# Optimization experiments

Hardware: AMD Instinct MI355X
Metric: run time of the kernel (lower is better)

Reference implementation:

```python
import jax, jax.numpy as jnp
import numpy as np

B, S, IN, H, T, OUT = 128, 336, 64, 1024, 96, 1


def _lstm_step(h, c, x, W_ih, W_hh, b_ih, b_hh):
    # PyTorch LSTM cell: gates in (i, f, g, o) order
    g = x @ W_ih.T + b_ih + h @ W_hh.T + b_hh  # [B, 4H]
    i, f, gg, o = jnp.split(g, 4, axis=-1)
    c_new = jax.nn.sigmoid(f) * c + jax.nn.sigmoid(i) * jnp.tanh(gg)
    h_new = jax.nn.sigmoid(o) * jnp.tanh(c_new)
    return h_new, c_new


def setup_inputs() -> dict:
    key = jax.random.key(0)
    ks = jax.random.split(key, 12)
    s = 0.05
    return {
        "src": jax.random.normal(ks[0], (B, S, IN), jnp.float32),
        "enc_W_ih": jax.random.normal(ks[1], (4 * H, IN), jnp.float32) * s,
        "enc_W_hh": jax.random.normal(ks[2], (4 * H, H), jnp.float32) * s,
        "enc_b_ih": jax.random.normal(ks[3], (4 * H,), jnp.float32) * s,
        "enc_b_hh": jax.random.normal(ks[4], (4 * H,), jnp.float32) * s,
        "dec_W_ih": jax.random.normal(ks[5], (4 * H, OUT + H), jnp.float32) * s,
        "dec_W_hh": jax.random.normal(ks[6], (4 * H, H), jnp.float32) * s,
        "dec_b_ih": jax.random.normal(ks[7], (4 * H,), jnp.float32) * s,
        "dec_b_hh": jax.random.normal(ks[8], (4 * H,), jnp.float32) * s,
        "attn_W": jax.random.normal(ks[9], (H, H), jnp.float32) * s,
        "fc_W": jax.random.normal(ks[10], (OUT, H), jnp.float32) * s,
        "fc_b": jax.random.normal(ks[11], (OUT,), jnp.float32) * s,
        "target_len": T,
    }


def reference(src, enc_W_ih, enc_W_hh, enc_b_ih, enc_b_hh,
              dec_W_ih, dec_W_hh, dec_b_ih, dec_b_hh,
              attn_W, fc_W, fc_b, target_len):
    batch = src.shape[0]
    hdim = enc_W_hh.shape[1]

    # ---- Encoder: single-layer LSTM over src, batch_first ----
    def enc_step(carry, x_t):
        h, c = carry
        h, c = _lstm_step(h, c, x_t, enc_W_ih, enc_W_hh, enc_b_ih, enc_b_hh)
        return (h, c), h

    h0 = jnp.zeros((batch, hdim), src.dtype)
    c0 = jnp.zeros((batch, hdim), src.dtype)
    (h_enc, c_enc), enc_hs = jax.lax.scan(enc_step, (h0, c0),
                                          jnp.swapaxes(src, 0, 1))
    encoder_outputs = jnp.swapaxes(enc_hs, 0, 1)  # [B, S, H]

    def dec_step(carry, _):
        h, c, prev_y = carry
        q = h @ attn_W.T                                      # [B, H]
        energy = jnp.einsum('bh,bsh->bs', q, encoder_outputs)  # [B, S]
        w = jax.nn.softmax(energy, axis=-1)
        ctx = jnp.einsum('bs,bsh->bh', w, encoder_outputs)     # [B, H]
        x = jnp.concatenate([prev_y, ctx], axis=-1)            # [B, OUT+H]
        h, c = _lstm_step(h, c, x, dec_W_ih, dec_W_hh, dec_b_ih, dec_b_hh)
        pred = h @ fc_W.T + fc_b                               # [B, OUT]
        prev_y = jax.lax.stop_gradient(pred)                   # pred.detach()
        return (h, c, prev_y), pred

    prev_y0 = jnp.zeros((batch, fc_W.shape[0]), src.dtype)
    _, preds = jax.lax.scan(dec_step, (h_enc, c_enc, prev_y0), None,
                            length=target_len)
    return jnp.swapaxes(preds, 0, 1)  # [B, target_len, OUT]
```

## Files before the change

kernel.cpp:

```cpp
#include <hip/hip_runtime.h>
#include <math.h>

#define Bn   128
#define Sn   336
#define INd  64
#define Hn   1024
#define Tn   96
#define G4   4096
#define KCE  34
#define KCD  65
#define KCQ  32

typedef __attribute__((ext_vector_type(8))) short short8;
typedef __attribute__((ext_vector_type(4))) float floatx4;
typedef __attribute__((ext_vector_type(4))) unsigned int uintx4;

__device__ __forceinline__ float sigmoidf_(float x){ return 1.0f/(1.0f+expf(-x)); }

__device__ __forceinline__ unsigned short f2bf(float f){
    union { float f; unsigned u; } v; v.f = f;
    unsigned r = v.u + 0x7fffu + ((v.u >> 16) & 1u);
    return (unsigned short)(r >> 16);
}
__device__ __forceinline__ float bflo(unsigned u){ union{unsigned u; float f;} v; v.u = u << 16;        return v.f; }
__device__ __forceinline__ float bfhi(unsigned u){ union{unsigned u; float f;} v; v.u = u & 0xffff0000u; return v.f; }
__device__ __forceinline__ void unpack8v(uintx4 v, float* f){
    f[0]=bflo(v.x); f[1]=bfhi(v.x); f[2]=bflo(v.y); f[3]=bfhi(v.y);
    f[4]=bflo(v.z); f[5]=bfhi(v.z); f[6]=bflo(v.w); f[7]=bfhi(v.w);
}

__global__ void pack_encf(const float* __restrict__ Wih, const float* __restrict__ Whh,
                          const float* __restrict__ bih, const float* __restrict__ bhh,
                          unsigned short* __restrict__ Wp, float* __restrict__ bc){
    long n = (long)256*KCE*512;
    for (long idx = (long)blockIdx.x*256 + threadIdx.x; idx < n; idx += (long)gridDim.x*256){
        int j = (int)(idx & 7), l = (int)((idx >> 3) & 63);
        int kc = (int)((idx >> 9) % KCE);
        int s  = (int)(idx / (KCE*512));
        int c = l & 15, kg = l >> 4;
        int k = kc*32 + kg*8 + j;
        int gate = s & 3, unit = (s >> 2)*16 + c;
        int orig = gate*Hn + unit;
        float v = (k < INd) ? Wih[orig*INd + k] : Whh[(size_t)orig*Hn + (k - INd)];
        Wp[idx] = f2bf(v);
    }
    int tid = blockIdx.x*256 + threadIdx.x;
    if (tid < G4){
        int g = (tid >> 4) & 3, u = (tid >> 6)*16 + (tid & 15);
        int orig = g*Hn + u;
        bc[tid] = bih[orig] + bhh[orig];
    }
}

__global__ void pack_decf(const float* __restrict__ Wih, const float* __restrict__ Whh,
                          const float* __restrict__ bih, const float* __restrict__ bhh,
                          unsigned short* __restrict__ Wp, float* __restrict__ bc){
    long n = (long)256*KCD*512;
    for (long idx = (long)blockIdx.x*256 + threadIdx.x; idx < n; idx += (long)gridDim.x*256){
        int j = (int)(idx & 7), l = (int)((idx >> 3) & 63);
        int kc = (int)((idx >> 9) % KCD);
        int s  = (int)(idx / (KCD*512));
        int c = l & 15, kg = l >> 4;
        int k = kc*32 + kg*8 + j;
        int gate = s & 3, unit = (s >> 2)*16 + c;
        int orig = gate*Hn + unit;
        float v;
        if (k < Hn)          v = Wih[(size_t)orig*(Hn+1) + 1 + k];
        else if (k < 2*Hn)   v = Whh[(size_t)orig*Hn + (k - Hn)];
        else if (k == 2*Hn)  v = Wih[(size_t)orig*(Hn+1)];
        else                 v = 0.0f;
        Wp[idx] = f2bf(v);
    }
    int tid = blockIdx.x*256 + threadIdx.x;
    if (tid < G4){
        int g = (tid >> 4) & 3, u = (tid >> 6)*16 + (tid & 15);
        int orig = g*Hn + u;
        bc[tid] = bih[orig] + bhh[orig];
    }
}

__global__ void pack_attnf(const float* __restrict__ w, unsigned short* __restrict__ Wp){
    int n = 64*KCQ*512;
    for (int idx = blockIdx.x*256 + threadIdx.x; idx < n; idx += gridDim.x*256){
        int j = idx & 7, l = (idx >> 3) & 63;
        int kc = (idx >> 9) & 31;
        int s  = idx >> 14;
        int nn = s*16 + (l & 15);
        int k = kc*32 + (l >> 4)*8 + j;
        Wp[idx] = f2bf(w[(size_t)nn*Hn + k]);
    }
}

__global__ void conv_srcf(const float* __restrict__ s, unsigned short* __restrict__ d){
    int n = Sn*8*2*512;
    for (int idx = blockIdx.x*256 + threadIdx.x; idx < n; idx += gridDim.x*256){
        int j = idx & 7, l = (idx >> 3) & 63;
        int kc = (idx >> 9) & 1, rg = (idx >> 10) & 7, t = idx >> 13;
        int b = rg*16 + (l & 15);
        int k = kc*32 + (l >> 4)*8 + j;
        d[idx] = f2bf(s[((size_t)b*Sn + t)*INd + k]);
    }
}

__global__ void init_ws(unsigned short* __restrict__ hf0, float* __restrict__ cbuf,
                        unsigned short* __restrict__ A0, unsigned short* __restrict__ A1){
    for (int i = blockIdx.x*256 + threadIdx.x; i < 8*KCD*512; i += gridDim.x*256){
        A0[i] = 0; A1[i] = 0;
        if (i < 8*32*512) hf0[i] = 0;
        if (i < Bn*Hn) cbuf[i] = 0.0f;
    }
}

__device__ __forceinline__ void swz(int b, int& x, int& y){
    int xcd = b & 7, li = b >> 3;
    y = xcd*8 + (li & 7);
    x = li >> 3;
}

__global__ __launch_bounds__(256)
void enc_step(const unsigned short* __restrict__ srcfrag,
              const unsigned short* __restrict__ hin,
              const unsigned short* __restrict__ Wf,
              const float* __restrict__ bc, float* __restrict__ cbuf,
              unsigned short* __restrict__ hout,
              unsigned short* __restrict__ enco,
              unsigned short* __restrict__ adec0,
              int t, int last)
{
    __shared__ float red[2][16][65];
    const int tid = threadIdx.x, l = tid & 63, w = tid >> 6;
    const int rgw = w & 1, kh = w >> 1;
    int x, y; swz(blockIdx.x, x, y);
    const int rg = x*2 + rgw;
    const int m0 = rg*16;
    const unsigned short* Bf = Wf + (size_t)(4*y)*KCE*512 + l*8;
    const unsigned short* Ax = srcfrag + ((size_t)t*8 + rg)*2*512 + l*8;
    const unsigned short* Ah = hin + (size_t)rg*32*512 + l*8;
    floatx4 acc0={0,0,0,0}, acc1={0,0,0,0}, acc2={0,0,0,0}, acc3={0,0,0,0};

    if (kh == 0){
        #pragma unroll
        for (int kc = 0; kc < 2; kc++){
            short8 a  = *(const short8*)(Ax + kc*512);
            short8 b0 = *(const short8*)(Bf + (0*KCE + kc)*512);
            short8 b1 = *(const short8*)(Bf + (1*KCE + kc)*512);
            short8 b2 = *(const short8*)(Bf + (2*KCE + kc)*512);
            short8 b3 = *(const short8*)(Bf + (3*KCE + kc)*512);
            acc0 = __builtin_amdgcn_mfma_f32_16x16x32_bf16(a, b0, acc0, 0, 0, 0);
            acc1 = __builtin_amdgcn_mfma_f32_16x16x32_bf16(a, b1, acc1, 0, 0, 0);
            acc2 = __builtin_amdgcn_mfma_f32_16x16x32_bf16(a, b2, acc2, 0, 0, 0);
            acc3 = __builtin_amdgcn_mfma_f32_16x16x32_bf16(a, b3, acc3, 0, 0, 0);
        }
        #pragma unroll 5
        for (int hc = 0; hc < 15; hc++){
            short8 a  = *(const short8*)(Ah + hc*512);
            short8 b0 = *(const short8*)(Bf + (0*KCE + hc + 2)*512);
            short8 b1 = *(const short8*)(Bf + (1*KCE + hc + 2)*512);
            short8 b2 = *(const short8*)(Bf + (2*KCE + hc + 2)*512);
            short8 b3 = *(const short8*)(Bf + (3*KCE + hc + 2)*512);
            acc0 = __builtin_amdgcn_mfma_f32_16x16x32_bf16(a, b0, acc0, 0, 0, 0);
            acc1 = __builtin_amdgcn_mfma_f32_16x16x32_bf16(a, b1, acc1, 0, 0, 0);
            acc2 = __builtin_amdgcn_mfma_f32_16x16x32_bf16(a, b2, acc2, 0, 0, 0);
            acc3 = __builtin_amdgcn_mfma_f32_16x16x32_bf16(a, b3, acc3, 0, 0, 0);
        }
    } else {
        #pragma unroll 5
        for (int hc = 15; hc < 32; hc++){
            short8 a  = *(const short8*)(Ah + hc*512);
            short8 b0 = *(const short8*)(Bf + (0*KCE + hc + 2)*512);
            short8 b1 = *(const short8*)(Bf + (1*KCE + hc + 2)*512);
            short8 b2 = *(const short8*)(Bf + (2*KCE + hc + 2)*512);
            short8 b3 = *(const short8*)(Bf + (3*KCE + hc + 2)*512);
            acc0 = __builtin_amdgcn_mfma_f32_16x16x32_bf16(a, b0, acc0, 0, 0, 0);
            acc1 = __builtin_amdgcn_mfma_f32_16x16x32_bf16(a, b1, acc1, 0, 0, 0);
            acc2 = __builtin_amdgcn_mfma_f32_16x16x32_bf16(a, b2, acc2, 0, 0, 0);
            acc3 = __builtin_amdgcn_mfma_f32_16x16x32_bf16(a, b3, acc3, 0, 0, 0);
        }
        #pragma unroll
        for (int r = 0; r < 4; r++){
            red[rgw][ 0 + r][l] = acc0[r];
            red[rgw][ 4 + r][l] = acc1[r];
            red[rgw][ 8 + r][l] = acc2[r];
            red[rgw][12 + r][l] = acc3[r];
        }
    }
    __syncthreads();
    if (kh != 0) return;
    #pragma unroll
    for (int r = 0; r < 4; r++){
        acc0[r] += red[rgw][ 0 + r][l];
        acc1[r] += red[rgw][ 4 + r][l];
        acc2[r] += red[rgw][ 8 + r][l];
        acc3[r] += red[rgw][12 + r][l];
    }

    const int col = l & 15, q = l >> 4;
    const int u = y*16 + col;
    const float bi  = bc[y*64 + col];
    const float bf_ = bc[y*64 + 16 + col];
    const float bg  = bc[y*64 + 32 + col];
    const float bo  = bc[y*64 + 48 + col];
    const int lsh = ((u >> 3) & 3) * 16;
    #pragma unroll
    for (int r = 0; r < 4; r++){
        const int m = m0 + q*4 + r;
        float gi = acc0[r] + bi;
        float gf = acc1[r] + bf_;
        float gg = acc2[r] + bg;
        float go = acc3[r] + bo;
        float co = cbuf[(size_t)m*Hn + u];
        float cn = sigmoidf_(gf)*co + sigmoidf_(gi)*tanhf(gg);
        float hv = sigmoidf_(go)*tanhf(cn);
        cbuf[(size_t)m*Hn + u] = cn;
        unsigned short hb = f2bf(hv);
        const int lanep = (q*4 + r) + lsh;
        hout[(((size_t)rg*32 + (u >> 5))*64 + lanep)*8 + (u & 7)] = hb;
        __builtin_nontemporal_store(hb, enco + ((size_t)m*Sn + t)*Hn + u);
        if (last) adec0[(((size_t)rg*KCD + 32 + (u >> 5))*64 + lanep)*8 + (u & 7)] = hb;
    }
}

__global__ __launch_bounds__(256)
void dec_step(const unsigned short* __restrict__ Ac,
              const unsigned short* __restrict__ Wf,
              const float* __restrict__ bc, float* __restrict__ cbuf,
              unsigned short* __restrict__ An)
{
    __shared__ float red[2][16][65];
    const int tid = threadIdx.x, l = tid & 63, w = tid >> 6;
    const int rgw = w & 1, kh = w >> 1;
    int x, y; swz(blockIdx.x, x, y);
    const int rg = x*2 + rgw;
    const int m0 = rg*16;
    const unsigned short* Bf = Wf + (size_t)(4*y)*KCD*512 + l*8;
    const unsigned short* Af = Ac + (size_t)rg*KCD*512 + l*8;
    floatx4 acc0={0,0,0,0}, acc1={0,0,0,0}, acc2={0,0,0,0}, acc3={0,0,0,0};

    const int k0 = kh ? 33 : 0;
    const int k1 = kh ? KCD : 33;
    #pragma unroll 5
    for (int kc = k0; kc < k1; kc++){
        short8 a  = *(const short8*)(Af + kc*512);
        short8 b0 = *(const short8*)(Bf + (0*KCD + kc)*512);
        short8 b1 = *(const short8*)(Bf + (1*KCD + kc)*512);
        short8 b2 = *(const short8*)(Bf + (2*KCD + kc)*512);
        short8 b3 = *(const short8*)(Bf + (3*KCD + kc)*512);
        acc0 = __builtin_amdgcn_mfma_f32_16x16x32_bf16(a, b0, acc0, 0, 0, 0);
        acc1 = __builtin_amdgcn_mfma_f32_16x16x32_bf16(a, b1, acc1, 0, 0, 0);
        acc2 = __builtin_amdgcn_mfma_f32_16x16x32_bf16(a, b2, acc2, 0, 0, 0);
        acc3 = __builtin_amdgcn_mfma_f32_16x16x32_bf16(a, b3, acc3, 0, 0, 0);
    }
    if (kh != 0){
        #pragma unroll
        for (int r = 0; r < 4; r++){
            red[rgw][ 0 + r][l] = acc0[r];
            red[rgw][ 4 + r][l] = acc1[r];
            red[rgw][ 8 + r][l] = acc2[r];
            red[rgw][12 + r][l] = acc3[r];
        }
    }
    __syncthreads();
    if (kh != 0) return;
    #pragma unroll
    for (int r = 0; r < 4; r++){
        acc0[r] += red[rgw][ 0 + r][l];
        acc1[r] += red[rgw][ 4 + r][l];
        acc2[r] += red[rgw][ 8 + r][l];
        acc3[r] += red[rgw][12 + r][l];
    }

    const int col = l & 15, q = l >> 4;
    const int u = y*16 + col;
    const float bi  = bc[y*64 + col];
    const float bf_ = bc[y*64 + 16 + col];
    const float bg  = bc[y*64 + 32 + col];
    const float bo  = bc[y*64 + 48 + col];
    const int lsh = ((u >> 3) & 3) * 16;
    #pragma unroll
    for (int r = 0; r < 4; r++){
        const int m = m0 + q*4 + r;
        float gi = acc0[r] + bi;
        float gf = acc1[r] + bf_;
        float gg = acc2[r] + bg;
        float go = acc3[r] + bo;
        float co = cbuf[(size_t)m*Hn + u];
        float cn = sigmoidf_(gf)*co + sigmoidf_(gi)*tanhf(gg);
        float hv = sigmoidf_(go)*tanhf(cn);
        cbuf[(size_t)m*Hn + u] = cn;
        const int lanep = (q*4 + r) + lsh;
        An[(((size_t)rg*KCD + 32 + (u >> 5))*64 + lanep)*8 + (u & 7)] = f2bf(hv);
    }
}

__global__ __launch_bounds__(256)
void attnq_step(const unsigned short* __restrict__ Ac, const unsigned short* __restrict__ Wf,
                unsigned short* __restrict__ qout)
{
    __shared__ float red[2][4][65];
    const int tid = threadIdx.x, l = tid & 63, w = tid >> 6;
    const int rgw = w & 1, kh = w >> 1;
    int x, y; swz(blockIdx.x, x, y);
    const int rg = x*2 + rgw;
    const int m0 = rg*16;
    const unsigned short* Bf = Wf + (size_t)y*KCQ*512 + l*8;
    const unsigned short* Af = Ac + ((size_t)rg*KCD + 32)*512 + l*8;
    floatx4 acc = {0,0,0,0};
    const int k0 = kh ? 16 : 0;
    const int k1 = kh ? 32 : 16;
    #pragma unroll 8
    for (int kc = k0; kc < k1; kc++){
        short8 a = *(const short8*)(Af + kc*512);
        short8 b = *(const short8*)(Bf + kc*512);
        acc = __builtin_amdgcn_mfma_f32_16x16x32_bf16(a, b, acc, 0, 0, 0);
    }
    if (kh != 0){
        #pragma unroll
        for (int r = 0; r < 4; r++) red[rgw][r][l] = acc[r];
    }
    __syncthreads();
    if (kh != 0) return;
    #pragma unroll
    for (int r = 0; r < 4; r++) acc[r] += red[rgw][r][l];

    const int col = l & 15, q = l >> 4;
    #pragma unroll
    for (int r = 0; r < 4; r++){
        const int m = m0 + q*4 + r;
        qout[(size_t)m*Hn + y*16 + col] = f2bf(acc[r]);
    }
}

__global__ __launch_bounds__(512)
void fattn_kernel(const unsigned short* __restrict__ q,
                  const unsigned short* __restrict__ enc,
                  unsigned short* __restrict__ Ac,
                  const float* __restrict__ fcW, const float* __restrict__ fcb,
                  float* __restrict__ out, int d)
{
    __shared__ float ctxl[8*1024];
    __shared__ float mred[8], lred[8];
    __shared__ float fcred[128];
    const int b = blockIdx.x;
    const int tid = threadIdx.x, w = tid >> 6, l = tid & 63;

    float qv[16];
    {
        const uintx4* qp = (const uintx4*)(q + (size_t)b*Hn) + l*2;
        uintx4 q0 = qp[0], q1 = qp[1];
        unpack8v(q0, qv); unpack8v(q1, qv + 8);
    }
    float m = -1e30f, lsum = 0.0f;
    float cacc[16];
    #pragma unroll
    for (int i = 0; i < 16; i++) cacc[i] = 0.0f;

    const uintx4* ebase = (const uintx4*)(enc + (size_t)b*Sn*Hn) + l*2;
    for (int s = w; s < Sn; s += 8){
        uintx4 e0 = __builtin_nontemporal_load(ebase + (size_t)s*128);
        uintx4 e1 = __builtin_nontemporal_load(ebase + (size_t)s*128 + 1);
        float ev[16];
        unpack8v(e0, ev); unpack8v(e1, ev + 8);
        float part = 0.0f;
        #pragma unroll
        for (int i = 0; i < 16; i++) part = fmaf(qv[i], ev[i], part);
        #pragma unroll
        for (int off = 32; off; off >>= 1) part += __shfl_down(part, off);
        float e = __shfl(part, 0);
        float mn = fmaxf(m, e);
        float corr = expf(m - mn);
        float p = expf(e - mn);
        lsum = lsum*corr + p;
        if (corr != 1.0f){
            #pragma unroll
            for (int i = 0; i < 16; i++) cacc[i] *= corr;
        }
        #pragma unroll
        for (int i = 0; i < 16; i++) cacc[i] = fmaf(p, ev[i], cacc[i]);
        m = mn;
    }
    if (l == 0){ mred[w] = m; lred[w] = lsum; }
    __syncthreads();
    float M = mred[0];
    #pragma unroll
    for (int k = 1; k < 8; k++) M = fmaxf(M, mred[k]);
    float corr = expf(m - M);
    #pragma unroll
    for (int j = 0; j < 16; j++) ctxl[w*1024 + j*64 + l] = cacc[j]*corr;
    __syncthreads();
    float L = 0.0f;
    #pragma unroll
    for (int k = 0; k < 8; k++) L += lred[k]*expf(mred[k] - M);
    float invL = 1.0f / L;

    {
        const int u0 = 2*tid;
        float s0 = 0.0f, s1 = 0.0f;
        #pragma unroll
        for (int k = 0; k < 8; k++){
            s0 += ctxl[k*1024 + (u0 & 15)*64 + (u0 >> 4)];
            s1 += ctxl[k*1024 + ((u0+1) & 15)*64 + ((u0+1) >> 4)];
        }
        ushort2 cv; cv.x = f2bf(s0*invL); cv.y = f2bf(s1*invL);
        const int kc = u0 >> 5;
        const int lanep = (b & 15) + ((u0 >> 3) & 3)*16;
        *(ushort2*)(Ac + ((((size_t)(b >> 4))*KCD + kc)*64 + lanep)*8 + (u0 & 7)) = cv;
    }

    float part = 0.0f;
    if (tid < 128){
        const unsigned short* hp = Ac + ((((size_t)(b >> 4))*KCD + 32 + (tid >> 2))*64
                                         + (b & 15) + (tid & 3)*16)*8;
        uintx4 hv = *(const uintx4*)hp;
        float hf[8]; unpack8v(hv, hf);
        #pragma unroll
        for (int j = 0; j < 8; j++) part = fmaf(hf[j], fcW[tid*8 + j], part);
    }
    __syncthreads();
    if (tid < 128) fcred[tid] = part;
    __syncthreads();
    for (int o = 64; o; o >>= 1){
        if (tid < o && tid + o < 128) fcred[tid] += fcred[tid + o];
        __syncthreads();
    }
    if (tid == 0 && d > 0){
        float p = fcred[0] + fcb[0];
        out[b*Tn + (d - 1)] = p;
        Ac[(((size_t)(b >> 4))*KCD + 64)*512 + (b & 15)*8] = f2bf(p);
    }
}

__global__ __launch_bounds__(128)
void fc_final(const unsigned short* __restrict__ A, const float* __restrict__ fcW,
              const float* __restrict__ fcb, float* __restrict__ out){
    __shared__ float red[128];
    const int b = blockIdx.x, tid = threadIdx.x;
    const unsigned short* hp = A + ((((size_t)(b >> 4))*KCD + 32 + (tid >> 2))*64
                                     + (b & 15) + (tid & 3)*16)*8;
    uintx4 hv = *(const uintx4*)hp;
    float hf[8]; unpack8v(hv, hf);
    float part = 0.0f;
    #pragma unroll
    for (int j = 0; j < 8; j++) part = fmaf(hf[j], fcW[tid*8 + j], part);
    red[tid] = part; __syncthreads();
    for (int o = 64; o; o >>= 1){
        if (tid < o) red[tid] += red[tid + o];
        __syncthreads();
    }
    if (tid == 0) out[b*Tn + (Tn - 1)] = red[0] + fcb[0];
}

extern "C" void kernel_launch(void* const* d_in, const int* in_sizes, int n_in,
                              void* d_out, int out_size, void* d_ws, size_t ws_size,
                              hipStream_t stream){
    const float* src  = (const float*)d_in[0];
    const float* eWih = (const float*)d_in[1];
    const float* eWhh = (const float*)d_in[2];
    const float* ebih = (const float*)d_in[3];
    const float* ebhh = (const float*)d_in[4];
    const float* dWih = (const float*)d_in[5];
    const float* dWhh = (const float*)d_in[6];
    const float* dbih = (const float*)d_in[7];
    const float* dbhh = (const float*)d_in[8];
    const float* attnW= (const float*)d_in[9];
    const float* fcW  = (const float*)d_in[10];
    const float* fcb  = (const float*)d_in[11];
    float* out = (float*)d_out;

    char* base = (char*)d_ws;
    auto alloc = [&](size_t bytes){ void* p = base; base += (bytes + 255) & ~255ull; return p; };
    unsigned short* Wencf = (unsigned short*)alloc((size_t)256*KCE*512*2);
    float*          benc  = (float*)alloc(G4*4);
    unsigned short* Wdecf = (unsigned short*)alloc((size_t)256*KCD*512*2);
    float*          bdec  = (float*)alloc(G4*4);
    unsigned short* Wattf = (unsigned short*)alloc((size_t)64*KCQ*512*2);
    unsigned short* srcf  = (unsigned short*)alloc((size_t)Sn*8*2*512*2);
    unsigned short* enco  = (unsigned short*)alloc((size_t)Bn*Sn*Hn*2);
    unsigned short* hf0   = (unsigned short*)alloc((size_t)8*32*512*2);
    unsigned short* hf1   = (unsigned short*)alloc((size_t)8*32*512*2);
    float*          cbuf  = (float*)alloc((size_t)Bn*Hn*4);
    unsigned short* A0f   = (unsigned short*)alloc((size_t)8*KCD*512*2);
    unsigned short* A1f   = (unsigned short*)alloc((size_t)8*KCD*512*2);
    unsigned short* qbf   = (unsigned short*)alloc((size_t)Bn*Hn*2);

    conv_srcf<<<2048, 256, 0, stream>>>(src, srcf);
    pack_encf<<<4096, 256, 0, stream>>>(eWih, eWhh, ebih, ebhh, Wencf, benc);
    pack_decf<<<8192, 256, 0, stream>>>(dWih, dWhh, dbih, dbhh, Wdecf, bdec);
    pack_attnf<<<1024, 256, 0, stream>>>(attnW, Wattf);
    init_ws<<<1040, 256, 0, stream>>>(hf0, cbuf, A0f, A1f);

    unsigned short* hf[2] = {hf0, hf1};
    unsigned short* Ad[2] = {A0f, A1f};

    for (int t = 0; t < Sn; t++){
        enc_step<<<256, 256, 0, stream>>>(srcf, hf[t&1], Wencf, benc, cbuf,
                                          hf[(t+1)&1], enco, A0f, t, t == Sn-1);
    }
    for (int d = 0; d < Tn; d++){
        unsigned short* Ac = Ad[d&1];
        unsigned short* An = Ad[(d+1)&1];
        attnq_step<<<256, 256, 0, stream>>>(Ac, Wattf, qbf);
        fattn_kernel<<<Bn, 512, 0, stream>>>(qbf, enco, Ac, fcW, fcb, out, d);
        dec_step<<<256, 256, 0, stream>>>(Ac, Wdecf, bdec, cbuf, An);
    }
    fc_final<<<Bn, 128, 0, stream>>>(Ad[0], fcW, fcb, out);
}
```

Before: 9.507 ms.

## Replace per-step launches with persistent cooperative encoder and decoder kernels

Turns the 336 encoder step launches and the 3×96 decoder launches into two persistent cooperative kernels that loop over time and use grid.sync between phases. The decoder kernel fuses the attention query, flash-style attention, LSTM step and fc projection, and splits the gate GEMM over four K-slices with an LDS reduction. The goal is to remove kernel launch overhead and inter-kernel gaps on a latency-bound recurrence. In exchange, every phase now waits on a grid-wide barrier, and residency of 256 blocks at 512 threads is required.

```diff
diff --git a/kernel.cpp b/kernel.cpp
--- a/kernel.cpp
+++ b/kernel.cpp
@@ -1,5 +1,8 @@
 #include <hip/hip_runtime.h>
+#include <hip/hip_cooperative_groups.h>
 #include <math.h>
+
+namespace cg = cooperative_groups;
 
 #define Bn   128
 #define Sn   336
@@ -117,16 +120,29 @@
     x = li >> 3;
 }
 
-__global__ __launch_bounds__(256)
-void enc_step(const unsigned short* __restrict__ srcfrag,
-              const unsigned short* __restrict__ hin,
+__device__ __forceinline__ float fcdot(const unsigned short* __restrict__ hplain,
+                                       const float* __restrict__ fcW, int b, int l){
+    const uintx4* hp = (const uintx4*)(hplain + (size_t)b*Hn) + l*2;
+    uintx4 h0 = hp[0], h1 = hp[1];
+    float hf[16]; unpack8v(h0, hf); unpack8v(h1, hf + 8);
+    float p = 0.0f;
+    #pragma unroll
+    for (int i = 0; i < 16; i++) p = fmaf(hf[i], fcW[l*16 + i], p);
+    #pragma unroll
+    for (int off = 32; off; off >>= 1) p += __shfl_down(p, off);
+    return p;
+}
+
+__global__ __launch_bounds__(256, 1)
+void enc_loop(const unsigned short* __restrict__ srcfrag,
               const unsigned short* __restrict__ Wf,
               const float* __restrict__ bc, float* __restrict__ cbuf,
-              unsigned short* __restrict__ hout,
+              unsigned short* __restrict__ hf0,
+              unsigned short* __restrict__ hf1,
               unsigned short* __restrict__ enco,
-              unsigned short* __restrict__ adec0,
-              int t, int last)
+              unsigned short* __restrict__ adec0)
 {
+    cg::grid_group grid = cg::this_grid();
     __shared__ float red[2][16][65];
     const int tid = threadIdx.x, l = tid & 63, w = tid >> 6;
     const int rgw = w & 1, kh = w >> 1;
@@ -134,65 +150,6 @@
     const int rg = x*2 + rgw;
     const int m0 = rg*16;
     const unsigned short* Bf = Wf + (size_t)(4*y)*KCE*512 + l*8;
-    const unsigned short* Ax = srcfrag + ((size_t)t*8 + rg)*2*512 + l*8;
-    const unsigned short* Ah = hin + (size_t)rg*32*512 + l*8;
-    floatx4 acc0={0,0,0,0}, acc1={0,0,0,0}, acc2={0,0,0,0}, acc3={0,0,0,0};
-
-    if (kh == 0){
-        #pragma unroll
-        for (int kc = 0; kc < 2; kc++){
-            short8 a  = *(const short8*)(Ax + kc*512);
-            short8 b0 = *(const short8*)(Bf + (0*KCE + kc)*512);
-            short8 b1 = *(const short8*)(Bf + (1*KCE + kc)*512);
-            short8 b2 = *(const short8*)(Bf + (2*KCE + kc)*512);
-            short8 b3 = *(const short8*)(Bf + (3*KCE + kc)*512);
-            acc0 = __builtin_amdgcn_mfma_f32_16x16x32_bf16(a, b0, acc0, 0, 0, 0);
-            acc1 = __builtin_amdgcn_mfma_f32_16x16x32_bf16(a, b1, acc1, 0, 0, 0);
-            acc2 = __builtin_amdgcn_mfma_f32_16x16x32_bf16(a, b2, acc2, 0, 0, 0);
-            acc3 = __builtin_amdgcn_mfma_f32_16x16x32_bf16(a, b3, acc3, 0, 0, 0);
-        }
-        #pragma unroll 5
-        for (int hc = 0; hc < 15; hc++){
-            short8 a  = *(const short8*)(Ah + hc*512);
-            short8 b0 = *(const short8*)(Bf + (0*KCE + hc + 2)*512);
-            short8 b1 = *(const short8*)(Bf + (1*KCE + hc + 2)*512);
-            short8 b2 = *(const short8*)(Bf + (2*KCE + hc + 2)*512);
-            short8 b3 = *(const short8*)(Bf + (3*KCE + hc + 2)*512);
-            acc0 = __builtin_amdgcn_mfma_f32_16x16x32_bf16(a, b0, acc0, 0, 0, 0);
-            acc1 = __builtin_amdgcn_mfma_f32_16x16x32_bf16(a, b1, acc1, 0, 0, 0);
-            acc2 = __builtin_amdgcn_mfma_f32_16x16x32_bf16(a, b2, acc2, 0, 0, 0);
-            acc3 = __builtin_amdgcn_mfma_f32_16x16x32_bf16(a, b3, acc3, 0, 0, 0);
-        }
-    } else {
-        #pragma unroll 5
-        for (int hc = 15; hc < 32; hc++){
-            short8 a  = *(const short8*)(Ah + hc*512);
-            short8 b0 = *(const short8*)(Bf + (0*KCE + hc + 2)*512);
-            short8 b1 = *(const short8*)(Bf + (1*KCE + hc + 2)*512);
-            short8 b2 = *(const short8*)(Bf + (2*KCE + hc + 2)*512);
-            short8 b3 = *(const short8*)(Bf + (3*KCE + hc + 2)*512);
-            acc0 = __builtin_amdgcn_mfma_f32_16x16x32_bf16(a, b0, acc0, 0, 0, 0);
-            acc1 = __builtin_amdgcn_mfma_f32_16x16x32_bf16(a, b1, acc1, 0, 0, 0);
-            acc2 = __builtin_amdgcn_mfma_f32_16x16x32_bf16(a, b2, acc2, 0, 0, 0);
-            acc3 = __builtin_amdgcn_mfma_f32_16x16x32_bf16(a, b3, acc3, 0, 0, 0);
-        }
-        #pragma unroll
-        for (int r = 0; r < 4; r++){
-            red[rgw][ 0 + r][l] = acc0[r];
-            red[rgw][ 4 + r][l] = acc1[r];
-            red[rgw][ 8 + r][l] = acc2[r];
-            red[rgw][12 + r][l] = acc3[r];
-        }
-    }
-    __syncthreads();
-    if (kh != 0) return;
-    #pragma unroll
-    for (int r = 0; r < 4; r++){
-        acc0[r] += red[rgw][ 0 + r][l];
-        acc1[r] += red[rgw][ 4 + r][l];
-        acc2[r] += red[rgw][ 8 + r][l];
-        acc3[r] += red[rgw][12 + r][l];
-    }
 
     const int col = l & 15, q = l >> 4;
     const int u = y*16 + col;
@@ -201,252 +158,307 @@
     const float bg  = bc[y*64 + 32 + col];
     const float bo  = bc[y*64 + 48 + col];
     const int lsh = ((u >> 3) & 3) * 16;
-    #pragma unroll
-    for (int r = 0; r < 4; r++){
-        const int m = m0 + q*4 + r;
-        float gi = acc0[r] + bi;
-        float gf = acc1[r] + bf_;
-        float gg = acc2[r] + bg;
-        float go = acc3[r] + bo;
-        float co = cbuf[(size_t)m*Hn + u];
-        float cn = sigmoidf_(gf)*co + sigmoidf_(gi)*tanhf(gg);
-        float hv = sigmoidf_(go)*tanhf(cn);
-        cbuf[(size_t)m*Hn + u] = cn;
-        unsigned short hb = f2bf(hv);
-        const int lanep = (q*4 + r) + lsh;
-        hout[(((size_t)rg*32 + (u >> 5))*64 + lanep)*8 + (u & 7)] = hb;
-        __builtin_nontemporal_store(hb, enco + ((size_t)m*Sn + t)*Hn + u);
-        if (last) adec0[(((size_t)rg*KCD + 32 + (u >> 5))*64 + lanep)*8 + (u & 7)] = hb;
-    }
-}
-
-__global__ __launch_bounds__(256)
-void dec_step(const unsigned short* __restrict__ Ac,
-              const unsigned short* __restrict__ Wf,
-              const float* __restrict__ bc, float* __restrict__ cbuf,
-              unsigned short* __restrict__ An)
+
+    for (int t = 0; t < Sn; t++){
+        const unsigned short* hin = (t & 1) ? hf1 : hf0;
+        unsigned short* hout      = (t & 1) ? hf0 : hf1;
+        const unsigned short* Ah = hin + (size_t)rg*32*512 + l*8;
+        floatx4 acc0={0,0,0,0}, acc1={0,0,0,0}, acc2={0,0,0,0}, acc3={0,0,0,0};
+
+        if (kh == 0){
+            const unsigned short* Ax = srcfrag + ((size_t)t*8 + rg)*2*512 + l*8;
+            #pragma unroll
+            for (int kc = 0; kc < 2; kc++){
+                short8 a  = *(const short8*)(Ax + kc*512);
+                short8 b0 = *(const short8*)(Bf + (0*KCE + kc)*512);
+                short8 b1 = *(const short8*)(Bf + (1*KCE + kc)*512);
+                short8 b2 = *(const short8*)(Bf + (2*KCE + kc)*512);
+                short8 b3 = *(const short8*)(Bf + (3*KCE + kc)*512);
+                acc0 = __builtin_amdgcn_mfma_f32_16x16x32_bf16(a, b0, acc0, 0, 0, 0);
+                acc1 = __builtin_amdgcn_mfma_f32_16x16x32_bf16(a, b1, acc1, 0, 0, 0);
+                acc2 = __builtin_amdgcn_mfma_f32_16x16x32_bf16(a, b2, acc2, 0, 0, 0);
+                acc3 = __builtin_amdgcn_mfma_f32_16x16x32_bf16(a, b3, acc3, 0, 0, 0);
+            }
+            #pragma unroll 5
+            for (int hc = 0; hc < 15; hc++){
+                short8 a  = *(const short8*)(Ah + hc*512);
+                short8 b0 = *(const short8*)(Bf + (0*KCE + hc + 2)*512);
+                short8 b1 = *(const short8*)(Bf + (1*KCE + hc + 2)*512);
+                short8 b2 = *(const short8*)(Bf + (2*KCE + hc + 2)*512);
+                short8 b3 = *(const short8*)(Bf + (3*KCE + hc + 2)*512);
+                acc0 = __builtin_amdgcn_mfma_f32_16x16x32_bf16(a, b0, acc0, 0, 0, 0);
+                acc1 = __builtin_amdgcn_mfma_f32_16x16x32_bf16(a, b1, acc1, 0, 0, 0);
+                acc2 = __builtin_amdgcn_mfma_f32_16x16x32_bf16(a, b2, acc2, 0, 0, 0);
+                acc3 = __builtin_amdgcn_mfma_f32_16x16x32_bf16(a, b3, acc3, 0, 0, 0);
+            }
+        } else {
+            #pragma unroll 5
+            for (int hc = 15; hc < 32; hc++){
+                short8 a  = *(const short8*)(Ah + hc*512);
+                short8 b0 = *(const short8*)(Bf + (0*KCE + hc + 2)*512);
+                short8 b1 = *(const short8*)(Bf + (1*KCE + hc + 2)*512);
+                short8 b2 = *(const short8*)(Bf + (2*KCE + hc + 2)*512);
+                short8 b3 = *(const short8*)(Bf + (3*KCE + hc + 2)*512);
+                acc0 = __builtin_amdgcn_mfma_f32_16x16x32_bf16(a, b0, acc0, 0, 0, 0);
+                acc1 = __builtin_amdgcn_mfma_f32_16x16x32_bf16(a, b1, acc1, 0, 0, 0);
+                acc2 = __builtin_amdgcn_mfma_f32_16x16x32_bf16(a, b2, acc2, 0, 0, 0);
+                acc3 = __builtin_amdgcn_mfma_f32_16x16x32_bf16(a, b3, acc3, 0, 0, 0);
+            }
+            #pragma unroll
+            for (int r = 0; r < 4; r++){
+                red[rgw][ 0 + r][l] = acc0[r];
+                red[rgw][ 4 + r][l] = acc1[r];
+                red[rgw][ 8 + r][l] = acc2[r];
+                red[rgw][12 + r][l] = acc3[r];
+            }
+        }
+        __syncthreads();
+        if (kh == 0){
+            #pragma unroll
+            for (int r = 0; r < 4; r++){
+                acc0[r] += red[rgw][ 0 + r][l];
+                acc1[r] += red[rgw][ 4 + r][l];
+                acc2[r] += red[rgw][ 8 + r][l];
+                acc3[r] += red[rgw][12 + r][l];
+            }
+            #pragma unroll
+            for (int r = 0; r < 4; r++){
+                const int m = m0 + q*4 + r;
+                float gi = acc0[r] + bi;
+                float gf = acc1[r] + bf_;
+                float gg = acc2[r] + bg;
+                float go = acc3[r] + bo;
+                float co = cbuf[(size_t)m*Hn + u];
+                float cn = sigmoidf_(gf)*co + sigmoidf_(gi)*tanhf(gg);
+                float hv = sigmoidf_(go)*tanhf(cn);
+                cbuf[(size_t)m*Hn + u] = cn;
+                unsigned short hb = f2bf(hv);
+                const int lanep = (q*4 + r) + lsh;
+                hout[(((size_t)rg*32 + (u >> 5))*64 + lanep)*8 + (u & 7)] = hb;
+                __builtin_nontemporal_store(hb, enco + ((size_t)m*Sn + t)*Hn + u);
+                if (t == Sn-1) adec0[(((size_t)rg*KCD + 32 + (u >> 5))*64 + lanep)*8 + (u & 7)] = hb;
+            }
+        }
+        grid.sync();
+    }
+}
+
+__global__ __launch_bounds__(512, 2)
+void dec_loop(unsigned short* __restrict__ A0, unsigned short* __restrict__ A1,
+              const unsigned short* __restrict__ Wdec,
+              const float* __restrict__ bdec, float* __restrict__ cbuf,
+              const unsigned short* __restrict__ Watt,
+              unsigned short* __restrict__ qbf,
+              const unsigned short* __restrict__ enco,
+              unsigned short* __restrict__ hplain,
+              const float* __restrict__ fcW, const float* __restrict__ fcb,
+              float* __restrict__ out)
 {
-    __shared__ float red[2][16][65];
+    cg::grid_group grid = cg::this_grid();
+    __shared__ float smem[8224];
     const int tid = threadIdx.x, l = tid & 63, w = tid >> 6;
-    const int rgw = w & 1, kh = w >> 1;
+    const int rgw = w & 1, ks = w >> 1;
     int x, y; swz(blockIdx.x, x, y);
-    const int rg = x*2 + rgw;
-    const int m0 = rg*16;
-    const unsigned short* Bf = Wf + (size_t)(4*y)*KCD*512 + l*8;
-    const unsigned short* Af = Ac + (size_t)rg*KCD*512 + l*8;
-    floatx4 acc0={0,0,0,0}, acc1={0,0,0,0}, acc2={0,0,0,0}, acc3={0,0,0,0};
-
-    const int k0 = kh ? 33 : 0;
-    const int k1 = kh ? KCD : 33;
-    #pragma unroll 5
-    for (int kc = k0; kc < k1; kc++){
-        short8 a  = *(const short8*)(Af + kc*512);
-        short8 b0 = *(const short8*)(Bf + (0*KCD + kc)*512);
-        short8 b1 = *(const short8*)(Bf + (1*KCD + kc)*512);
-        short8 b2 = *(const short8*)(Bf + (2*KCD + kc)*512);
-        short8 b3 = *(const short8*)(Bf + (3*KCD + kc)*512);
-        acc0 = __builtin_amdgcn_mfma_f32_16x16x32_bf16(a, b0, acc0, 0, 0, 0);
-        acc1 = __builtin_amdgcn_mfma_f32_16x16x32_bf16(a, b1, acc1, 0, 0, 0);
-        acc2 = __builtin_amdgcn_mfma_f32_16x16x32_bf16(a, b2, acc2, 0, 0, 0);
-        acc3 = __builtin_amdgcn_mfma_f32_16x16x32_bf16(a, b3, acc3, 0, 0, 0);
-    }
-    if (kh != 0){
-        #pragma unroll
-        for (int r = 0; r < 4; r++){
-            red[rgw][ 0 + r][l] = acc0[r];
-            red[rgw][ 4 + r][l] = acc1[r];
-            red[rgw][ 8 + r][l] = acc2[r];
-            red[rgw][12 + r][l] = acc3[r];
-        }
-    }
-    __syncthreads();
-    if (kh != 0) return;
-    #pragma unroll
-    for (int r = 0; r < 4; r++){
-        acc0[r] += red[rgw][ 0 + r][l];
-        acc1[r] += red[rgw][ 4 + r][l];
-        acc2[r] += red[rgw][ 8 + r][l];
-        acc3[r] += red[rgw][12 + r][l];
-    }
-
-    const int col = l & 15, q = l >> 4;
+    const int rg = x*2 + rgw, m0 = rg*16;
+    const unsigned short* Bf = Wdec + (size_t)(4*y)*KCD*512 + l*8;
+
+    const int col = l & 15, q4 = l >> 4;
     const int u = y*16 + col;
-    const float bi  = bc[y*64 + col];
-    const float bf_ = bc[y*64 + 16 + col];
-    const float bg  = bc[y*64 + 32 + col];
-    const float bo  = bc[y*64 + 48 + col];
+    const float bi  = bdec[y*64 + col];
+    const float bf_ = bdec[y*64 + 16 + col];
+    const float bg  = bdec[y*64 + 32 + col];
+    const float bo  = bdec[y*64 + 48 + col];
     const int lsh = ((u >> 3) & 3) * 16;
-    #pragma unroll
-    for (int r = 0; r < 4; r++){
-        const int m = m0 + q*4 + r;
-        float gi = acc0[r] + bi;
-        float gf = acc1[r] + bf_;
-        float gg = acc2[r] + bg;
-        float go = acc3[r] + bo;
-        float co = cbuf[(size_t)m*Hn + u];
-        float cn = sigmoidf_(gf)*co + sigmoidf_(gi)*tanhf(gg);
-        float hv = sigmoidf_(go)*tanhf(cn);
-        cbuf[(size_t)m*Hn + u] = cn;
-        const int lanep = (q*4 + r) + lsh;
-        An[(((size_t)rg*KCD + 32 + (u >> 5))*64 + lanep)*8 + (u & 7)] = f2bf(hv);
-    }
-}
-
-__global__ __launch_bounds__(256)
-void attnq_step(const unsigned short* __restrict__ Ac, const unsigned short* __restrict__ Wf,
-                unsigned short* __restrict__ qout)
-{
-    __shared__ float red[2][4][65];
-    const int tid = threadIdx.x, l = tid & 63, w = tid >> 6;
-    const int rgw = w & 1, kh = w >> 1;
-    int x, y; swz(blockIdx.x, x, y);
-    const int rg = x*2 + rgw;
-    const int m0 = rg*16;
-    const unsigned short* Bf = Wf + (size_t)y*KCQ*512 + l*8;
-    const unsigned short* Af = Ac + ((size_t)rg*KCD + 32)*512 + l*8;
-    floatx4 acc = {0,0,0,0};
-    const int k0 = kh ? 16 : 0;
-    const int k1 = kh ? 32 : 16;
-    #pragma unroll 8
-    for (int kc = k0; kc < k1; kc++){
-        short8 a = *(const short8*)(Af + kc*512);
-        short8 b = *(const short8*)(Bf + kc*512);
-        acc = __builtin_amdgcn_mfma_f32_16x16x32_bf16(a, b, acc, 0, 0, 0);
-    }
-    if (kh != 0){
-        #pragma unroll
-        for (int r = 0; r < 4; r++) red[rgw][r][l] = acc[r];
-    }
-    __syncthreads();
-    if (kh != 0) return;
-    #pragma unroll
-    for (int r = 0; r < 4; r++) acc[r] += red[rgw][r][l];
-
-    const int col = l & 15, q = l >> 4;
-    #pragma unroll
-    for (int r = 0; r < 4; r++){
-        const int m = m0 + q*4 + r;
-        qout[(size_t)m*Hn + y*16 + col] = f2bf(acc[r]);
-    }
-}
-
-__global__ __launch_bounds__(512)
-void fattn_kernel(const unsigned short* __restrict__ q,
-                  const unsigned short* __restrict__ enc,
-                  unsigned short* __restrict__ Ac,
-                  const float* __restrict__ fcW, const float* __restrict__ fcb,
-                  float* __restrict__ out, int d)
-{
-    __shared__ float ctxl[8*1024];
-    __shared__ float mred[8], lred[8];
-    __shared__ float fcred[128];
-    const int b = blockIdx.x;
-    const int tid = threadIdx.x, w = tid >> 6, l = tid & 63;
-
-    float qv[16];
-    {
-        const uintx4* qp = (const uintx4*)(q + (size_t)b*Hn) + l*2;
-        uintx4 q0 = qp[0], q1 = qp[1];
-        unpack8v(q0, qv); unpack8v(q1, qv + 8);
-    }
-    float m = -1e30f, lsum = 0.0f;
-    float cacc[16];
-    #pragma unroll
-    for (int i = 0; i < 16; i++) cacc[i] = 0.0f;
-
-    const uintx4* ebase = (const uintx4*)(enc + (size_t)b*Sn*Hn) + l*2;
-    for (int s = w; s < Sn; s += 8){
-        uintx4 e0 = __builtin_nontemporal_load(ebase + (size_t)s*128);
-        uintx4 e1 = __builtin_nontemporal_load(ebase + (size_t)s*128 + 1);
-        float ev[16];
-        unpack8v(e0, ev); unpack8v(e1, ev + 8);
-        float part = 0.0f;
-        #pragma unroll
-        for (int i = 0; i < 16; i++) part = fmaf(qv[i], ev[i], part);
-        #pragma unroll
-        for (int off = 32; off; off >>= 1) part += __shfl_down(part, off);
-        float e = __shfl(part, 0);
-        float mn = fmaxf(m, e);
-        float corr = expf(m - mn);
-        float p = expf(e - mn);
-        lsum = lsum*corr + p;
-        if (corr != 1.0f){
-            #pragma unroll
-            for (int i = 0; i < 16; i++) cacc[i] *= corr;
-        }
-        #pragma unroll
-        for (int i = 0; i < 16; i++) cacc[i] = fmaf(p, ev[i], cacc[i]);
-        m = mn;
-    }
-    if (l == 0){ mred[w] = m; lred[w] = lsum; }
-    __syncthreads();
-    float M = mred[0];
-    #pragma unroll
-    for (int k = 1; k < 8; k++) M = fmaxf(M, mred[k]);
-    float corr = expf(m - M);
-    #pragma unroll
-    for (int j = 0; j < 16; j++) ctxl[w*1024 + j*64 + l] = cacc[j]*corr;
-    __syncthreads();
-    float L = 0.0f;
-    #pragma unroll
-    for (int k = 0; k < 8; k++) L += lred[k]*expf(mred[k] - M);
-    float invL = 1.0f / L;
-
-    {
-        const int u0 = 2*tid;
-        float s0 = 0.0f, s1 = 0.0f;
-        #pragma unroll
-        for (int k = 0; k < 8; k++){
-            s0 += ctxl[k*1024 + (u0 & 15)*64 + (u0 >> 4)];
-            s1 += ctxl[k*1024 + ((u0+1) & 15)*64 + ((u0+1) >> 4)];
-        }
-        ushort2 cv; cv.x = f2bf(s0*invL); cv.y = f2bf(s1*invL);
-        const int kc = u0 >> 5;
-        const int lanep = (b & 15) + ((u0 >> 3) & 3)*16;
-        *(ushort2*)(Ac + ((((size_t)(b >> 4))*KCD + kc)*64 + lanep)*8 + (u0 & 7)) = cv;
-    }
-
-    float part = 0.0f;
-    if (tid < 128){
-        const unsigned short* hp = Ac + ((((size_t)(b >> 4))*KCD + 32 + (tid >> 2))*64
-                                         + (b & 15) + (tid & 3)*16)*8;
-        uintx4 hv = *(const uintx4*)hp;
-        float hf[8]; unpack8v(hv, hf);
-        #pragma unroll
-        for (int j = 0; j < 8; j++) part = fmaf(hf[j], fcW[tid*8 + j], part);
-    }
-    __syncthreads();
-    if (tid < 128) fcred[tid] = part;
-    __syncthreads();
-    for (int o = 64; o; o >>= 1){
-        if (tid < o && tid + o < 128) fcred[tid] += fcred[tid + o];
+
+    for (int d = 0; d < Tn; d++){
+        unsigned short* Ac = (d & 1) ? A1 : A0;
+        unsigned short* An = (d & 1) ? A0 : A1;
+        const unsigned short* Af = Ac + (size_t)rg*KCD*512 + l*8;
+
+        floatx4 acc0={0,0,0,0}, acc1={0,0,0,0}, acc2={0,0,0,0}, acc3={0,0,0,0};
+        {
+            const int kc0 = 32 + ks*8;
+            #pragma unroll
+            for (int kk = 0; kk < 8; kk++){
+                const int kc = kc0 + kk;
+                short8 a  = *(const short8*)(Af + kc*512);
+                short8 b0 = *(const short8*)(Bf + (0*KCD + kc)*512);
+                short8 b1 = *(const short8*)(Bf + (1*KCD + kc)*512);
+                short8 b2 = *(const short8*)(Bf + (2*KCD + kc)*512);
+                short8 b3 = *(const short8*)(Bf + (3*KCD + kc)*512);
+                acc0 = __builtin_amdgcn_mfma_f32_16x16x32_bf16(a, b0, acc0, 0, 0, 0);
+                acc1 = __builtin_amdgcn_mfma_f32_16x16x32_bf16(a, b1, acc1, 0, 0, 0);
+                acc2 = __builtin_amdgcn_mfma_f32_16x16x32_bf16(a, b2, acc2, 0, 0, 0);
+                acc3 = __builtin_amdgcn_mfma_f32_16x16x32_bf16(a, b3, acc3, 0, 0, 0);
+            }
+        }
+        if (ks == 1){
+            const unsigned short* Aq = Ac + ((size_t)rg*KCD + 32)*512 + l*8;
+            const unsigned short* Bq = Watt + (size_t)y*KCQ*512 + l*8;
+            floatx4 qa = {0,0,0,0};
+            #pragma unroll 8
+            for (int kc = 0; kc < KCQ; kc++){
+                short8 a = *(const short8*)(Aq + kc*512);
+                short8 b = *(const short8*)(Bq + kc*512);
+                qa = __builtin_amdgcn_mfma_f32_16x16x32_bf16(a, b, qa, 0, 0, 0);
+            }
+            #pragma unroll
+            for (int r = 0; r < 4; r++)
+                qbf[(size_t)(m0 + q4*4 + r)*Hn + y*16 + col] = f2bf(qa[r]);
+        }
+        if (d > 0 && x == 0 && w >= 6){
+            const int b = y*2 + (w & 1);
+            float p = fcdot(hplain, fcW, b, l);
+            if (l == 0){
+                float pv = p + fcb[0];
+                out[b*Tn + (d-1)] = pv;
+                Ac[(((size_t)(b >> 4))*KCD + 64)*512 + (b & 15)*8] = f2bf(pv);
+            }
+        }
+        grid.sync();
+
+        if (blockIdx.x < Bn){
+            const int b = blockIdx.x;
+            float* ctxl = smem;
+            float* mred = smem + 8192;
+            float* lred = smem + 8200;
+            float qv[16];
+            {
+                const uintx4* qp = (const uintx4*)(qbf + (size_t)b*Hn) + l*2;
+                uintx4 q0 = qp[0], q1 = qp[1];
+                unpack8v(q0, qv); unpack8v(q1, qv + 8);
+            }
+            float mx = -1e30f, lsum = 0.0f;
+            float cacc[16];
+            #pragma unroll
+            for (int i = 0; i < 16; i++) cacc[i] = 0.0f;
+
+            const uintx4* ebase = (const uintx4*)(enco + (size_t)b*Sn*Hn) + l*2;
+            for (int s = w; s < Sn; s += 8){
+                uintx4 e0 = __builtin_nontemporal_load(ebase + (size_t)s*128);
+                uintx4 e1 = __builtin_nontemporal_load(ebase + (size_t)s*128 + 1);
+                float ev[16];
+                unpack8v(e0, ev); unpack8v(e1, ev + 8);
+                float part = 0.0f;
+                #pragma unroll
+                for (int i = 0; i < 16; i++) part = fmaf(qv[i], ev[i], part);
+                #pragma unroll
+                for (int off = 32; off; off >>= 1) part += __shfl_down(part, off);
+                float e = __shfl(part, 0);
+                float mn = fmaxf(mx, e);
+                float corr = expf(mx - mn);
+                float p = expf(e - mn);
+                lsum = lsum*corr + p;
+                if (corr != 1.0f){
+                    #pragma unroll
+                    for (int i = 0; i < 16; i++) cacc[i] *= corr;
+                }
+                #pragma unroll
+                for (int i = 0; i < 16; i++) cacc[i] = fmaf(p, ev[i], cacc[i]);
+                mx = mn;
+            }
+            if (l == 0){ mred[w] = mx; lred[w] = lsum; }
+            __syncthreads();
+            float M = mred[0];
+            #pragma unroll
+            for (int k = 1; k < 8; k++) M = fmaxf(M, mred[k]);
+            float corr2 = expf(mx - M);
+            #pragma unroll
+            for (int j = 0; j < 16; j++) ctxl[w*1024 + j*64 + l] = cacc[j]*corr2;
+            __syncthreads();
+            float L = 0.0f;
+            #pragma unroll
+            for (int k = 0; k < 8; k++) L += lred[k]*expf(mred[k] - M);
+            float invL = 1.0f / L;
+
+            const int u0 = 2*tid;
+            float s0 = 0.0f, s1 = 0.0f;
+            #pragma unroll
+            for (int k = 0; k < 8; k++){
+                s0 += ctxl[k*1024 + (u0 & 15)*64 + (u0 >> 4)];
+                s1 += ctxl[k*1024 + ((u0+1) & 15)*64 + ((u0+1) >> 4)];
+            }
+            ushort2 cv; cv.x = f2bf(s0*invL); cv.y = f2bf(s1*invL);
+            const int kcw = u0 >> 5;
+            const int lanep2 = (b & 15) + ((u0 >> 3) & 3)*16;
+            *(ushort2*)(Ac + ((((size_t)(b >> 4))*KCD + kcw)*64 + lanep2)*8 + (u0 & 7)) = cv;
+        }
+        grid.sync();
+
+        {
+            const int kc0 = ks*8;
+            #pragma unroll
+            for (int kk = 0; kk < 8; kk++){
+                const int kc = kc0 + kk;
+                short8 a  = *(const short8*)(Af + kc*512);
+                short8 b0 = *(const short8*)(Bf + (0*KCD + kc)*512);
+                short8 b1 = *(const short8*)(Bf + (1*KCD + kc)*512);
+                short8 b2 = *(const short8*)(Bf + (2*KCD + kc)*512);
+                short8 b3 = *(const short8*)(Bf + (3*KCD + kc)*512);
+                acc0 = __builtin_amdgcn_mfma_f32_16x16x32_bf16(a, b0, acc0, 0, 0, 0);
+                acc1 = __builtin_amdgcn_mfma_f32_16x16x32_bf16(a, b1, acc1, 0, 0, 0);
+                acc2 = __builtin_amdgcn_mfma_f32_16x16x32_bf16(a, b2, acc2, 0, 0, 0);
+                acc3 = __builtin_amdgcn_mfma_f32_16x16x32_bf16(a, b3, acc3, 0, 0, 0);
+            }
+            if (ks == 3){
+                short8 a  = *(const short8*)(Af + 64*512);
+                short8 b0 = *(const short8*)(Bf + (0*KCD + 64)*512);
+                short8 b1 = *(const short8*)(Bf + (1*KCD + 64)*512);
+                short8 b2 = *(const short8*)(Bf + (2*KCD + 64)*512);
+                short8 b3 = *(const short8*)(Bf + (3*KCD + 64)*512);
+                acc0 = __builtin_amdgcn_mfma_f32_16x16x32_bf16(a, b0, acc0, 0, 0, 0);
+                acc1 = __builtin_amdgcn_mfma_f32_16x16x32_bf16(a, b1, acc1, 0, 0, 0);
+                acc2 = __builtin_amdgcn_mfma_f32_16x16x32_bf16(a, b2, acc2, 0, 0, 0);
+                acc3 = __builtin_amdgcn_mfma_f32_16x16x32_bf16(a, b3, acc3, 0, 0, 0);
+            }
+        }
+        if (ks != 0){
+            float* rp = smem + ((ks-1)*2 + rgw)*1024;
+            #pragma unroll
+            for (int r = 0; r < 4; r++){
+                rp[( 0 + r)*64 + l] = acc0[r];
+                rp[( 4 + r)*64 + l] = acc1[r];
+                rp[( 8 + r)*64 + l] = acc2[r];
+                rp[(12 + r)*64 + l] = acc3[r];
+            }
+        }
         __syncthreads();
-    }
-    if (tid == 0 && d > 0){
-        float p = fcred[0] + fcb[0];
-        out[b*Tn + (d - 1)] = p;
-        Ac[(((size_t)(b >> 4))*KCD + 64)*512 + (b & 15)*8] = f2bf(p);
-    }
-}
-
-__global__ __launch_bounds__(128)
-void fc_final(const unsigned short* __restrict__ A, const float* __restrict__ fcW,
-              const float* __restrict__ fcb, float* __restrict__ out){
-    __shared__ float red[128];
-    const int b = blockIdx.x, tid = threadIdx.x;
-    const unsigned short* hp = A + ((((size_t)(b >> 4))*KCD + 32 + (tid >> 2))*64
-                                     + (b & 15) + (tid & 3)*16)*8;
-    uintx4 hv = *(const uintx4*)hp;
-    float hf[8]; unpack8v(hv, hf);
-    float part = 0.0f;
-    #pragma unroll
-    for (int j = 0; j < 8; j++) part = fmaf(hf[j], fcW[tid*8 + j], part);
-    red[tid] = part; __syncthreads();
-    for (int o = 64; o; o >>= 1){
-        if (tid < o) red[tid] += red[tid + o];
-        __syncthreads();
-    }
-    if (tid == 0) out[b*Tn + (Tn - 1)] = red[0] + fcb[0];
+        if (ks == 0){
+            const float* r0 = smem + rgw*1024;
+            const float* r1 = smem + (2 + rgw)*1024;
+            const float* r2 = smem + (4 + rgw)*1024;
+            #pragma unroll
+            for (int r = 0; r < 4; r++){
+                acc0[r] += r0[( 0+r)*64 + l] + r1[( 0+r)*64 + l] + r2[( 0+r)*64 + l];
+                acc1[r] += r0[( 4+r)*64 + l] + r1[( 4+r)*64 + l] + r2[( 4+r)*64 + l];
+                acc2[r] += r0[( 8+r)*64 + l] + r1[( 8+r)*64 + l] + r2[( 8+r)*64 + l];
+                acc3[r] += r0[(12+r)*64 + l] + r1[(12+r)*64 + l] + r2[(12+r)*64 + l];
+            }
+            #pragma unroll
+            for (int r = 0; r < 4; r++){
+                const int m = m0 + q4*4 + r;
+                float gi = acc0[r] + bi;
+                float gf = acc1[r] + bf_;
+                float gg = acc2[r] + bg;
+                float go = acc3[r] + bo;
+                float co = cbuf[(size_t)m*Hn + u];
+                float cn = sigmoidf_(gf)*co + sigmoidf_(gi)*tanhf(gg);
+                float hv = sigmoidf_(go)*tanhf(cn);
+                cbuf[(size_t)m*Hn + u] = cn;
+                unsigned short hb = f2bf(hv);
+                const int lanep = (q4*4 + r) + lsh;
+                An[(((size_t)rg*KCD + 32 + (u >> 5))*64 + lanep)*8 + (u & 7)] = hb;
+                hplain[(size_t)m*Hn + u] = hb;
+            }
+        }
+        grid.sync();
+    }
+
+    if (x == 0 && w >= 6){
+        const int b = y*2 + (w & 1);
+        float p = fcdot(hplain, fcW, b, l);
+        if (l == 0) out[b*Tn + (Tn - 1)] = p + fcb[0];
+    }
 }
 
 extern "C" void kernel_launch(void* const* d_in, const int* in_sizes, int n_in,
@@ -481,6 +493,7 @@
     unsigned short* A0f   = (unsigned short*)alloc((size_t)8*KCD*512*2);
     unsigned short* A1f   = (unsigned short*)alloc((size_t)8*KCD*512*2);
     unsigned short* qbf   = (unsigned short*)alloc((size_t)Bn*Hn*2);
+    unsigned short* hplain= (unsigned short*)alloc((size_t)Bn*Hn*2);
 
     conv_srcf<<<2048, 256, 0, stream>>>(src, srcf);
     pack_encf<<<4096, 256, 0, stream>>>(eWih, eWhh, ebih, ebhh, Wencf, benc);
@@ -488,19 +501,15 @@
     pack_attnf<<<1024, 256, 0, stream>>>(attnW, Wattf);
     init_ws<<<1040, 256, 0, stream>>>(hf0, cbuf, A0f, A1f);
 
-    unsigned short* hf[2] = {hf0, hf1};
-    unsigned short* Ad[2] = {A0f, A1f};
-
-    for (int t = 0; t < Sn; t++){
-        enc_step<<<256, 256, 0, stream>>>(srcf, hf[t&1], Wencf, benc, cbuf,
-                                          hf[(t+1)&1], enco, A0f, t, t == Sn-1);
-    }
-    for (int d = 0; d < Tn; d++){
-        unsigned short* Ac = Ad[d&1];
-        unsigned short* An = Ad[(d+1)&1];
-        attnq_step<<<256, 256, 0, stream>>>(Ac, Wattf, qbf);
-        fattn_kernel<<<Bn, 512, 0, stream>>>(qbf, enco, Ac, fcW, fcb, out, d);
-        dec_step<<<256, 256, 0, stream>>>(Ac, Wdecf, bdec, cbuf, An);
-    }
-    fc_final<<<Bn, 128, 0, stream>>>(Ad[0], fcW, fcb, out);
-}
+    {
+        void* ea[] = {(void*)&srcf, (void*)&Wencf, (void*)&benc, (void*)&cbuf,
+                      (void*)&hf0, (void*)&hf1, (void*)&enco, (void*)&A0f};
+        hipLaunchCooperativeKernel(enc_loop, dim3(256), dim3(256), ea, 0, stream);
+    }
+    {
+        void* da[] = {(void*)&A0f, (void*)&A1f, (void*)&Wdecf, (void*)&bdec, (void*)&cbuf,
+                      (void*)&Wattf, (void*)&qbf, (void*)&enco, (void*)&hplain,
+                      (void*)&fcW, (void*)&fcb, (void*)&out};
+        hipLaunchCooperativeKernel(dec_loop, dim3(256), dim3(512), da, 0, stream);
+    }
+}
```

After: 27.84 ms. 2.93x slower.
